# Optimization experiments

Measured on AMD Instinct MI355X. Metric: run time of the kernel, lower is better.

Reference implementation:

```python
import jax, jax.numpy as jnp
import numpy as np

B, S, H, K = 64, 512, 768, 64
NR, NN, ND = 9, 3, 3


def setup_inputs() -> dict:
    key = jax.random.key(0)
    ks = jax.random.split(key, 20)
    inp = {}
    inp["sequence_output"] = jax.random.normal(ks[0], (B, S, H), jnp.float32)
    for i, name in enumerate(["rel", "nov", "dir"]):
        inp[f"{name}_idx"] = jax.random.randint(ks[1 + i], (B, K), 0, S)
        inp[f"{name}_len"] = jax.random.randint(ks[4 + i], (B,), 0, K + 1)
    scale = 0.02
    for i, (name, nlab) in enumerate([("rel", NR), ("nov", NN), ("dir", ND)]):
        k0, k1 = jax.random.split(ks[7 + i])
        inp[f"{name}_dense_W"] = scale * jax.random.normal(k0, (H, H), jnp.float32)
        inp[f"{name}_dense_b"] = jnp.zeros((H,), jnp.float32)
        inp[f"{name}_cls_W"] = scale * jax.random.normal(k1, (nlab, H), jnp.float32)
        inp[f"{name}_cls_b"] = jnp.zeros((nlab,), jnp.float32)
    return inp


def _attn_pool(seq, idx, length):
    """Ragged intra-group self-attention pooling (get_token_reps / get_ne_reps).

    seq: [B,S,H]; idx: [B,K] padded token indices; length: [B] valid counts.
    Original computes (softmax(G G^T) @ G)[0]; only row 0 of the attention is
    needed, so we compute just that row.
    """
    G = jnp.take_along_axis(seq, idx[:, :, None], axis=1)  # [B,K,H]
    mask = jnp.arange(idx.shape[1])[None, :] < length[:, None]  # [B,K]
    scores0 = jnp.einsum('bh,bjh->bj', G[:, 0], G)  # row 0 of G G^T
    scores0 = jnp.where(mask, scores0, jnp.float32(-1e30))
    a0 = jax.nn.softmax(scores0, axis=-1)  # [B,K]
    pooled = jnp.einsum('bj,bjh->bh', a0, G)  # [B,H]
    # empty-group fallback: sequence_output[b, 0]
    return jnp.where(length[:, None] > 0, pooled, seq[:, 0])


def _head(rep, Wd, bd, Wc, bc):
    # HiddenTokenPooler dense + tanh, then token classifier
    h = jnp.tanh(rep @ Wd.T + bd)
    return h @ Wc.T + bc


def reference(sequence_output, rel_idx, rel_len, nov_idx, nov_len, dir_idx, dir_len,
              rel_dense_W, rel_dense_b, rel_cls_W, rel_cls_b,
              nov_dense_W, nov_dense_b, nov_cls_W, nov_cls_b,
              dir_dense_W, dir_dense_b, dir_cls_W, dir_cls_b):
    rel_rep = _attn_pool(sequence_output, rel_idx, rel_len)
    nov_rep = _attn_pool(sequence_output, nov_idx, nov_len)
    dir_rep = _attn_pool(sequence_output, dir_idx, dir_len)
    rel_logits = _head(rel_rep, rel_dense_W, rel_dense_b, rel_cls_W, rel_cls_b)
    nov_logits = _head(nov_rep, nov_dense_W, nov_dense_b, nov_cls_W, nov_cls_b)
    dir_logits = _head(dir_rep, dir_dense_W, dir_dense_b, dir_cls_W, dir_cls_b)
    return (rel_logits, nov_logits, dir_logits)
```

## Files before the change

### kernel.cpp

```cpp
#include <hip/hip_runtime.h>
#include <math.h>


#define Hdim 768
#define Kdim 64
#define Sdim 512
#define Bdim 64
#define LDK  72

typedef float f32x4 __attribute__((ext_vector_type(4)));
typedef short bf16x8 __attribute__((ext_vector_type(8)));

__device__ __forceinline__ unsigned short f2bf(float f) {
    union { float f; unsigned int u; } c; c.f = f;
    unsigned int u = c.u + 0x7FFFu + ((c.u >> 16) & 1u);
    return (unsigned short)(u >> 16);
}

__global__ __launch_bounds__(1024) void k_pool(
    const float* __restrict__ seq,
    const int* __restrict__ idxr, const int* __restrict__ lenr,
    const int* __restrict__ idxn, const int* __restrict__ lenn,
    const int* __restrict__ idxd, const int* __restrict__ lend,
    const float* __restrict__ cbr, const float* __restrict__ cbn,
    const float* __restrict__ cbd,
    float* __restrict__ pooled,
    float* __restrict__ out)
{
    const int b = blockIdx.x, g = blockIdx.y;
    const int tid = threadIdx.x, lane = tid & 63, wave = tid >> 6;

    const int* idxp = (g == 0) ? idxr : (g == 1) ? idxn : idxd;
    const int* lnp  = (g == 0) ? lenr : (g == 1) ? lenn : lend;

    __shared__ int   sidx[Kdim];
    __shared__ float wm[16], wl[16], coef[16];
    __shared__ float wpart[16][Hdim];

    if (tid < Kdim) sidx[tid] = idxp[b * Kdim + tid];
    const int len = lnp[b];

    if (b == 0) {
        if (g == 0)      { if (tid < 576) out[tid]       = cbr[tid % 9]; }
        else if (g == 1) { if (tid < 192) out[576 + tid] = cbn[tid % 3]; }
        else             { if (tid < 192) out[768 + tid] = cbd[tid % 3]; }
    }
    __syncthreads();

    float* dst = pooled + ((size_t)g * Bdim + b) * Hdim;

    if (len > 0) {
        const float* row0 = seq + ((size_t)b * Sdim + sidx[0]) * Hdim;
        float g0[12];
#pragma unroll
        for (int k = 0; k < 3; ++k) {
            float4 v = *(const float4*)(row0 + 4 * lane + 256 * k);
            g0[4 * k + 0] = v.x; g0[4 * k + 1] = v.y;
            g0[4 * k + 2] = v.z; g0[4 * k + 3] = v.w;
        }

        float m = -1e30f, l = 0.f;
        float p[12] = {0,0,0,0,0,0,0,0,0,0,0,0};

        for (int j = wave; j < len; j += 16) {
            const float* rowj = seq + ((size_t)b * Sdim + sidx[j]) * Hdim;
            float v[12];
#pragma unroll
            for (int k = 0; k < 3; ++k) {
                float4 t = *(const float4*)(rowj + 4 * lane + 256 * k);
                v[4 * k + 0] = t.x; v[4 * k + 1] = t.y;
                v[4 * k + 2] = t.z; v[4 * k + 3] = t.w;
            }
            float s = 0.f;
#pragma unroll
            for (int k = 0; k < 12; ++k) s += g0[k] * v[k];
#pragma unroll
            for (int off = 32; off > 0; off >>= 1) s += __shfl_xor(s, off, 64);

            float mn    = fmaxf(m, s);
            float scale = __expf(m - mn);
            float e     = __expf(s - mn);
            l = l * scale + e;
#pragma unroll
            for (int k = 0; k < 12; ++k) p[k] = p[k] * scale + e * v[k];
            m = mn;
        }

        if (lane == 0) { wm[wave] = m; wl[wave] = l; }
#pragma unroll
        for (int k = 0; k < 3; ++k)
            *(float4*)&wpart[wave][4 * lane + 256 * k] =
                make_float4(p[4 * k], p[4 * k + 1], p[4 * k + 2], p[4 * k + 3]);
        __syncthreads();

        if (wave == 0 && lane < 16) {
            float mw = wm[lane], lw = wl[lane];
            float M = mw;
#pragma unroll
            for (int off = 8; off > 0; off >>= 1) M = fmaxf(M, __shfl_xor(M, off, 64));
            float sc = __expf(mw - M);
            float Ls = lw * sc;
#pragma unroll
            for (int off = 8; off > 0; off >>= 1) Ls += __shfl_xor(Ls, off, 64);
            coef[lane] = sc / Ls;
        }
        __syncthreads();

        if (tid < Hdim) {
            float acc = 0.f;
#pragma unroll
            for (int w = 0; w < 16; ++w) acc += wpart[w][tid] * coef[w];
            dst[tid] = acc;
        }
    } else {
        if (tid < Hdim) dst[tid] = seq[(size_t)b * Sdim * Hdim + tid];
    }
}

__global__ __launch_bounds__(256) void k_dense_cls(
    const float* __restrict__ pooled,
    const float* __restrict__ dWr, const float* __restrict__ dbr,
    const float* __restrict__ cWr,
    const float* __restrict__ dWn, const float* __restrict__ dbn,
    const float* __restrict__ cWn,
    const float* __restrict__ dWd, const float* __restrict__ dbd,
    const float* __restrict__ cWd,
    float* __restrict__ out)
{
    const int mt = blockIdx.x, g = blockIdx.y;
    const float *dW, *db, *cW; int nlab, off;
    if (g == 0)      { dW = dWr; db = dbr; cW = cWr; nlab = 9; off = 0;   }
    else if (g == 1) { dW = dWn; db = dbn; cW = cWn; nlab = 3; off = 576; }
    else             { dW = dWd; db = dbd; cW = cWd; nlab = 3; off = 768; }
    const int i0 = mt * 64;

    const int tid = threadIdx.x, lane = tid & 63, wv = tid >> 6;
    const int q = lane >> 4, col = lane & 15;

    __shared__ unsigned short Ws[64 * LDK];
    __shared__ unsigned short Ps[64 * LDK];
    __shared__ float hs[64][65];

    f32x4 acc[4] = {{0,0,0,0},{0,0,0,0},{0,0,0,0},{0,0,0,0}};

    const int srow  = tid >> 2;
    const int cbase = (tid & 3) * 16;
    const float* Pg = pooled + (size_t)g * Bdim * Hdim;

    for (int kk = 0; kk < Hdim; kk += 64) {
#pragma unroll
        for (int u = 0; u < 4; ++u) {
            int c = cbase + 4 * u;
            float4 w4 = *(const float4*)(dW + (size_t)(i0 + srow) * Hdim + kk + c);
            float4 p4 = *(const float4*)(Pg + (size_t)srow * Hdim + kk + c);
            *(ushort4*)&Ws[srow * LDK + c] = make_ushort4(f2bf(w4.x), f2bf(w4.y), f2bf(w4.z), f2bf(w4.w));
            *(ushort4*)&Ps[srow * LDK + c] = make_ushort4(f2bf(p4.x), f2bf(p4.y), f2bf(p4.z), f2bf(p4.w));
        }
        __syncthreads();
#pragma unroll
        for (int ks = 0; ks < 64; ks += 32) {
            bf16x8 a = *(const bf16x8*)&Ws[(wv * 16 + col) * LDK + ks + 8 * q];
#pragma unroll
            for (int n = 0; n < 4; ++n) {
                bf16x8 bb = *(const bf16x8*)&Ps[(n * 16 + col) * LDK + ks + 8 * q];
                acc[n] = __builtin_amdgcn_mfma_f32_16x16x32_bf16(a, bb, acc[n], 0, 0, 0);
            }
        }
        __syncthreads();
    }

#pragma unroll
    for (int n = 0; n < 4; ++n) {
        int bb = n * 16 + col;
#pragma unroll
        for (int r = 0; r < 4; ++r) {
            int il = wv * 16 + q * 4 + r;
            hs[il][bb] = tanhf(acc[n][r] + db[i0 + il]);
        }
    }
    __syncthreads();

    for (int c = wv; c < nlab; c += 4) {
        const float* wr = cW + (size_t)c * Hdim + i0;
        float a = 0.f;
#pragma unroll 16
        for (int il = 0; il < 64; ++il)
            a += wr[il] * hs[il][lane];
        atomicAdd(&out[off + lane * nlab + c], a);
    }
}

extern "C" void kernel_launch(void* const* d_in, const int* in_sizes, int n_in,
                              void* d_out, int out_size, void* d_ws, size_t ws_size,
                              hipStream_t stream) {
    const float* seq  = (const float*)d_in[0];
    const int*   idxr = (const int*)d_in[1];
    const int*   lenr = (const int*)d_in[2];
    const int*   idxn = (const int*)d_in[3];
    const int*   lenn = (const int*)d_in[4];
    const int*   idxd = (const int*)d_in[5];
    const int*   lend = (const int*)d_in[6];
    const float* dWr  = (const float*)d_in[7];
    const float* dbr  = (const float*)d_in[8];
    const float* cWr  = (const float*)d_in[9];
    const float* cbr  = (const float*)d_in[10];
    const float* dWn  = (const float*)d_in[11];
    const float* dbn  = (const float*)d_in[12];
    const float* cWn  = (const float*)d_in[13];
    const float* cbn  = (const float*)d_in[14];
    const float* dWd  = (const float*)d_in[15];
    const float* dbd  = (const float*)d_in[16];
    const float* cWd  = (const float*)d_in[17];
    const float* cbd  = (const float*)d_in[18];
    float* out = (float*)d_out;

    float* pooled = (float*)d_ws;

    k_pool<<<dim3(Bdim, 3), 1024, 0, stream>>>(
        seq, idxr, lenr, idxn, lenn, idxd, lend, cbr, cbn, cbd, pooled, out);
    k_dense_cls<<<dim3(Hdim / 64, 3), 256, 0, stream>>>(
        pooled, dWr, dbr, cWr, dWn, dbn, cWn, dWd, dbd, cWd, out);
}
```

Measured before the change: 189.1 us.

## Convert dense weights and pooled reps to bf16 in pool kernel, stream MFMA operands directly

The dense weights' fp32-to-bf16 conversion moves into the pooling kernel, spread across all pool blocks, and the pooled vectors are now written as bf16. The dense kernel then loads MFMA operands straight from global memory, with no LDS staging or per-tile barriers. The aim is to take the conversion and synchronisation off the small 36-block dense kernel's critical path and to halve its input bytes. The cost is extra global writes and reads of bf16 weights in the pool kernel, plus uncoalesced strided global operand loads in the dense kernel.

```diff
diff --git a/kernel.cpp b/kernel.cpp
--- a/kernel.cpp
+++ b/kernel.cpp
@@ -6,7 +6,6 @@
 #define Kdim 64
 #define Sdim 512
 #define Bdim 64
-#define LDK  72
 
 typedef float f32x4 __attribute__((ext_vector_type(4)));
 typedef short bf16x8 __attribute__((ext_vector_type(8)));
@@ -15,6 +14,13 @@
     union { float f; unsigned int u; } c; c.f = f;
     unsigned int u = c.u + 0x7FFFu + ((c.u >> 16) & 1u);
     return (unsigned short)(u >> 16);
+}
+
+__device__ __forceinline__ void cvt8(const float* __restrict__ src,
+                                     unsigned short* __restrict__ dst) {
+    float4 x = *(const float4*)src, y = *(const float4*)(src + 4);
+    *(ushort4*)dst       = make_ushort4(f2bf(x.x), f2bf(x.y), f2bf(x.z), f2bf(x.w));
+    *(ushort4*)(dst + 4) = make_ushort4(f2bf(y.x), f2bf(y.y), f2bf(y.z), f2bf(y.w));
 }
 
 __global__ __launch_bounds__(1024) void k_pool(
@@ -24,7 +30,10 @@
     const int* __restrict__ idxd, const int* __restrict__ lend,
     const float* __restrict__ cbr, const float* __restrict__ cbn,
     const float* __restrict__ cbd,
-    float* __restrict__ pooled,
+    const float* __restrict__ dWr, const float* __restrict__ dWn,
+    const float* __restrict__ dWd,
+    unsigned short* __restrict__ Wbf,
+    unsigned short* __restrict__ Pbf,
     float* __restrict__ out)
 {
     const int b = blockIdx.x, g = blockIdx.y;
@@ -47,7 +56,7 @@
     }
     __syncthreads();
 
-    float* dst = pooled + ((size_t)g * Bdim + b) * Hdim;
+    unsigned short* Pb = Pbf + ((size_t)g * Bdim + b) * Hdim;
 
     if (len > 0) {
         const float* row0 = seq + ((size_t)b * Sdim + sidx[0]) * Hdim;
@@ -110,65 +119,55 @@
             float acc = 0.f;
 #pragma unroll
             for (int w = 0; w < 16; ++w) acc += wpart[w][tid] * coef[w];
-            dst[tid] = acc;
+            Pb[tid] = f2bf(acc);
         }
     } else {
-        if (tid < Hdim) dst[tid] = seq[(size_t)b * Sdim * Hdim + tid];
+        if (tid < Hdim) Pb[tid] = f2bf(seq[(size_t)b * Sdim * Hdim + tid]);
+    }
+
+    {
+        const float* dW = (g == 0) ? dWr : (g == 1) ? dWn : dWd;
+        unsigned short* Wb = Wbf + (size_t)g * Hdim * Hdim;
+        for (int e = (b * 1024 + tid) * 8; e < Hdim * Hdim; e += 64 * 1024 * 8)
+            cvt8(dW + e, Wb + e);
     }
 }
 
 __global__ __launch_bounds__(256) void k_dense_cls(
-    const float* __restrict__ pooled,
-    const float* __restrict__ dWr, const float* __restrict__ dbr,
-    const float* __restrict__ cWr,
-    const float* __restrict__ dWn, const float* __restrict__ dbn,
-    const float* __restrict__ cWn,
-    const float* __restrict__ dWd, const float* __restrict__ dbd,
+    const unsigned short* __restrict__ Wbf,
+    const unsigned short* __restrict__ Pbf,
+    const float* __restrict__ dbr, const float* __restrict__ dbn,
+    const float* __restrict__ dbd,
+    const float* __restrict__ cWr, const float* __restrict__ cWn,
     const float* __restrict__ cWd,
     float* __restrict__ out)
 {
     const int mt = blockIdx.x, g = blockIdx.y;
-    const float *dW, *db, *cW; int nlab, off;
-    if (g == 0)      { dW = dWr; db = dbr; cW = cWr; nlab = 9; off = 0;   }
-    else if (g == 1) { dW = dWn; db = dbn; cW = cWn; nlab = 3; off = 576; }
-    else             { dW = dWd; db = dbd; cW = cWd; nlab = 3; off = 768; }
+    const float *db, *cW; int nlab, off;
+    if (g == 0)      { db = dbr; cW = cWr; nlab = 9; off = 0;   }
+    else if (g == 1) { db = dbn; cW = cWn; nlab = 3; off = 576; }
+    else             { db = dbd; cW = cWd; nlab = 3; off = 768; }
     const int i0 = mt * 64;
 
     const int tid = threadIdx.x, lane = tid & 63, wv = tid >> 6;
     const int q = lane >> 4, col = lane & 15;
 
-    __shared__ unsigned short Ws[64 * LDK];
-    __shared__ unsigned short Ps[64 * LDK];
+    const unsigned short* Ap = Wbf + ((size_t)g * Hdim + i0 + wv * 16 + col) * Hdim + 8 * q;
+    const unsigned short* Bp = Pbf + ((size_t)g * Bdim + col) * Hdim + 8 * q;
+
+    f32x4 acc[4] = {{0,0,0,0},{0,0,0,0},{0,0,0,0},{0,0,0,0}};
+
+#pragma unroll 6
+    for (int ks = 0; ks < Hdim; ks += 32) {
+        bf16x8 a = *(const bf16x8*)(Ap + ks);
+#pragma unroll
+        for (int n = 0; n < 4; ++n) {
+            bf16x8 bb = *(const bf16x8*)(Bp + (size_t)n * 16 * Hdim + ks);
+            acc[n] = __builtin_amdgcn_mfma_f32_16x16x32_bf16(a, bb, acc[n], 0, 0, 0);
+        }
+    }
+
     __shared__ float hs[64][65];
-
-    f32x4 acc[4] = {{0,0,0,0},{0,0,0,0},{0,0,0,0},{0,0,0,0}};
-
-    const int srow  = tid >> 2;
-    const int cbase = (tid & 3) * 16;
-    const float* Pg = pooled + (size_t)g * Bdim * Hdim;
-
-    for (int kk = 0; kk < Hdim; kk += 64) {
-#pragma unroll
-        for (int u = 0; u < 4; ++u) {
-            int c = cbase + 4 * u;
-            float4 w4 = *(const float4*)(dW + (size_t)(i0 + srow) * Hdim + kk + c);
-            float4 p4 = *(const float4*)(Pg + (size_t)srow * Hdim + kk + c);
-            *(ushort4*)&Ws[srow * LDK + c] = make_ushort4(f2bf(w4.x), f2bf(w4.y), f2bf(w4.z), f2bf(w4.w));
-            *(ushort4*)&Ps[srow * LDK + c] = make_ushort4(f2bf(p4.x), f2bf(p4.y), f2bf(p4.z), f2bf(p4.w));
-        }
-        __syncthreads();
-#pragma unroll
-        for (int ks = 0; ks < 64; ks += 32) {
-            bf16x8 a = *(const bf16x8*)&Ws[(wv * 16 + col) * LDK + ks + 8 * q];
-#pragma unroll
-            for (int n = 0; n < 4; ++n) {
-                bf16x8 bb = *(const bf16x8*)&Ps[(n * 16 + col) * LDK + ks + 8 * q];
-                acc[n] = __builtin_amdgcn_mfma_f32_16x16x32_bf16(a, bb, acc[n], 0, 0, 0);
-            }
-        }
-        __syncthreads();
-    }
-
 #pragma unroll
     for (int n = 0; n < 4; ++n) {
         int bb = n * 16 + col;
@@ -214,10 +213,12 @@
     const float* cbd  = (const float*)d_in[18];
     float* out = (float*)d_out;
 
-    float* pooled = (float*)d_ws;
+    unsigned short* Wbf = (unsigned short*)d_ws;
+    unsigned short* Pbf = Wbf + (size_t)3 * Hdim * Hdim;
 
     k_pool<<<dim3(Bdim, 3), 1024, 0, stream>>>(
-        seq, idxr, lenr, idxn, lenn, idxd, lend, cbr, cbn, cbd, pooled, out);
+        seq, idxr, lenr, idxn, lenn, idxd, lend,
+        cbr, cbn, cbd, dWr, dWn, dWd, Wbf, Pbf, out);
     k_dense_cls<<<dim3(Hdim / 64, 3), 256, 0, stream>>>(
-        pooled, dWr, dbr, cWr, dWn, dbn, cWn, dWd, dbd, cWd, out);
-}
+        Wbf, Pbf, dbr, dbn, dbd, cWr, cWn, cWd, out);
+}
```

Result: no change. 189.8 us (+0.4%).
